# Kernel optimization log

Measured on AMD Instinct MI355X. Metric: run time of the kernel, lower is better.

## Reference

```python
import jax, jax.numpy as jnp
import numpy as np

NUM_STAB = 0.001  # numerical_stabilizer from relu_kernel_transformation


def relu_kernel(data, proj):
    """ReLU random-feature kernel: data [B,L,H,D], proj [M,D] -> [B,L,H,M]."""
    ratio = 1.0 / jnp.sqrt(jnp.asarray(proj.shape[0], jnp.float32))
    data_dash = ratio * jnp.einsum('blhd,md->blhm', data, proj)
    return jax.nn.relu(data_dash) + NUM_STAB


def setup_inputs() -> dict:
    key = jax.random.key(0)
    k1, k2, k3, k4 = jax.random.split(key, 4)
    B, L, H, D, M = 2, 4096, 8, 64, 256
    return {
        'query': jax.random.normal(k1, (B, L, H, D), jnp.float32),
        'key_t': jax.random.normal(k2, (B, L, H, D), jnp.float32),
        'value': jax.random.normal(k3, (B, L, H, D), jnp.float32),
        'projection_matrix': jax.random.normal(k4, (M, D), jnp.float32),
    }


def reference(query, key_t, value, projection_matrix):
    # Kernel feature maps [B,L,H,M]
    qp = relu_kernel(query, projection_matrix)
    kp = relu_kernel(key_t, projection_matrix)
    # Causal path operates in [L,B,H,*] layout
    qs = jnp.transpose(qp, (1, 0, 2, 3))     # [L,B,H,M]
    ks = jnp.transpose(kp, (1, 0, 2, 3))     # [L,B,H,M]
    vs = jnp.transpose(value, (1, 0, 2, 3))  # [L,B,H,D]

    B, H, M = qs.shape[1], qs.shape[2], qs.shape[3]
    D = vs.shape[3]
    init = (jnp.zeros((B, H, M, D), qs.dtype),  # running sum of k outer v
            jnp.zeros((B, H, M), qs.dtype))     # running sum of k

    def step(carry, inp):
        kv_sum, k_sum = carry
        q, k, v = inp  # [B,H,M], [B,H,M], [B,H,D]
        kv_sum = kv_sum + k[..., None] * v[..., None, :]
        k_sum = k_sum + k
        num = jnp.einsum('bhmd,bhm->bhd', kv_sum, q)  # causal numerator step
        den = jnp.einsum('bhm,bhm->bh', q, k_sum)     # causal denominator step
        return (kv_sum, k_sum), (num, den)

    _, (num, den) = jax.lax.scan(step, init, (qs, ks, vs))  # num [L,B,H,D], den [L,B,H]
    den = den[..., None]
    den = jnp.where(den <= 0.0, jnp.ones_like(den), den)
    out = num / den                      # [L,B,H,D]
    return jnp.transpose(out, (1, 0, 2, 3))  # [B,L,H,D]
```

## Files before the change

kernel.cpp:

```cpp
#include <hip/hip_runtime.h>
#include <hip/hip_bf16.h>


#define B_   2
#define L_   4096
#define H_   8
#define D_   64
#define M_   256
#define T_   128
#define C_   (L_ / T_)
#define NBH  (B_ * H_)
#define RATIO 0.0625f
#define STAB  0.001f
#define SVT  136
#define SQS  72

typedef __attribute__((ext_vector_type(8))) short short8;
typedef __attribute__((ext_vector_type(4))) float floatx4;

#define MFMA16(a, b, c) __builtin_amdgcn_mfma_f32_16x16x32_bf16(a, b, c, 0, 0, 0)

__device__ inline unsigned short f2bf(float x) {
    union { float f; unsigned u; } v; v.f = x;
    unsigned r = v.u + 0x7FFF + ((v.u >> 16) & 1);
    return (unsigned short)(r >> 16);
}
__device__ inline unsigned pack2bf(float a, float b) {
    __hip_bfloat162 h = __float22bfloat162_rn(make_float2(a, b));
    unsigned u; __builtin_memcpy(&u, &h, 4);
    return u;
}
__device__ inline short8 ldg8_bfs(const float* p) {
    float4 a = *(const float4*)p;
    float4 b = *(const float4*)(p + 4);
    short8 r;
    r[0] = (short)f2bf(a.x * RATIO); r[1] = (short)f2bf(a.y * RATIO);
    r[2] = (short)f2bf(a.z * RATIO); r[3] = (short)f2bf(a.w * RATIO);
    r[4] = (short)f2bf(b.x * RATIO); r[5] = (short)f2bf(b.y * RATIO);
    r[6] = (short)f2bf(b.z * RATIO); r[7] = (short)f2bf(b.w * RATIO);
    return r;
}

__global__ __launch_bounds__(256, 2)
void prep_kernel(const float* __restrict__ val, const float* __restrict__ proj,
                 unsigned short* __restrict__ VTg, unsigned short* __restrict__ Pbf) {
    const int c = blockIdx.x, bh = blockIdx.y;
    const int b = bh / H_, h = bh % H_;
    const int tid = threadIdx.x;
    __shared__ __align__(16) unsigned short VT[64 * SVT];

    const size_t rowstr = H_ * D_;
    const size_t base = ((size_t)b * L_ + (size_t)c * T_) * rowstr + (size_t)h * D_;

    for (int i = tid; i < T_ * 16; i += 256) {
        int t = i >> 4, d4 = (i & 15) * 4;
        float4 vv = *(const float4*)(val + base + (size_t)t * rowstr + d4);
        VT[(d4 + 0) * SVT + t] = f2bf(vv.x);
        VT[(d4 + 1) * SVT + t] = f2bf(vv.y);
        VT[(d4 + 2) * SVT + t] = f2bf(vv.z);
        VT[(d4 + 3) * SVT + t] = f2bf(vv.w);
    }
    __syncthreads();
    unsigned short* vout = VTg + ((size_t)bh * C_ + c) * (D_ * T_);
    for (int i = tid; i < D_ * 16; i += 256) {
        int d = i >> 4, tt = (i & 15) * 8;
        *(uint4*)(vout + d * T_ + tt) = *(const uint4*)&VT[d * SVT + tt];
    }
    if (c == 0) {
        int i = bh * 256 + tid;
        float4 pv = *(const float4*)(proj + (size_t)i * 4);
        uint2 o; o.x = pack2bf(pv.x, pv.y); o.y = pack2bf(pv.z, pv.w);
        *(uint2*)(Pbf + (size_t)i * 4) = o;
    }
}

__global__ __launch_bounds__(512, 1)
void scan_kernel(const float* __restrict__ key,
                 const unsigned short* __restrict__ VTg,
                 const unsigned short* __restrict__ Pbf,
                 unsigned short* __restrict__ S, float* __restrict__ Z) {
    const int mq = blockIdx.x, bh = blockIdx.y, dh = blockIdx.z;
    const int b = bh / H_, h = bh % H_;
    const int tid = threadIdx.x;
    const int w = tid >> 6, lane = tid & 63;
    const int l15 = lane & 15, quad = lane >> 4;

    __shared__ __align__(16) unsigned short KpT[2][32 * SVT];
    __shared__ float zP[2][4][32];

    const size_t rowstr = H_ * D_;
    const size_t khead = (size_t)b * L_ * rowstr + (size_t)h * D_;

    if (w < 4) {
        short8 pf[2][2];
#pragma unroll
        for (int ct = 0; ct < 2; ++ct)
#pragma unroll
            for (int kk = 0; kk < 2; ++kk)
                pf[ct][kk] = *(const short8*)(Pbf + (size_t)(mq * 32 + ct * 16 + l15) * D_
                                              + kk * 32 + quad * 8);
        short8 kf[2][2];
#pragma unroll
        for (int rt = 0; rt < 2; ++rt)
#pragma unroll
            for (int kk = 0; kk < 2; ++kk)
                kf[rt][kk] = ldg8_bfs(key + khead
                                      + (size_t)(32 * w + rt * 16 + l15) * rowstr
                                      + kk * 32 + quad * 8);
#pragma unroll
        for (int ct = 0; ct < 2; ++ct) {
            float zpart = 0.f;
#pragma unroll
            for (int rt = 0; rt < 2; ++rt) {
                floatx4 a = {0.f, 0.f, 0.f, 0.f};
                a = MFMA16(kf[rt][0], pf[ct][0], a);
                a = MFMA16(kf[rt][1], pf[ct][1], a);
                float k0 = fmaxf(a[0], 0.f) + STAB;
                float k1 = fmaxf(a[1], 0.f) + STAB;
                float k2 = fmaxf(a[2], 0.f) + STAB;
                float k3 = fmaxf(a[3], 0.f) + STAB;
                zpart += (k0 + k1) + (k2 + k3);
                uint2 pk; pk.x = pack2bf(k0, k1); pk.y = pack2bf(k2, k3);
                *(uint2*)&KpT[0][(ct * 16 + l15) * SVT + 32 * w + rt * 16 + quad * 4] = pk;
            }
            zpart += __shfl_xor(zpart, 16, 64);
            zpart += __shfl_xor(zpart, 32, 64);
            if (quad == 0) zP[0][w][ct * 16 + l15] = zpart;
        }
#pragma unroll
        for (int rt = 0; rt < 2; ++rt)
#pragma unroll
            for (int kk = 0; kk < 2; ++kk)
                kf[rt][kk] = ldg8_bfs(key + khead + (size_t)T_ * rowstr
                                      + (size_t)(32 * w + rt * 16 + l15) * rowstr
                                      + kk * 32 + quad * 8);
        __syncthreads();
        for (int c = 0; c < C_; ++c) {
            const int buf = c & 1;
            if (c + 1 < C_) {
#pragma unroll
                for (int ct = 0; ct < 2; ++ct) {
                    float zpart = 0.f;
#pragma unroll
                    for (int rt = 0; rt < 2; ++rt) {
                        floatx4 a = {0.f, 0.f, 0.f, 0.f};
                        a = MFMA16(kf[rt][0], pf[ct][0], a);
                        a = MFMA16(kf[rt][1], pf[ct][1], a);
                        float k0 = fmaxf(a[0], 0.f) + STAB;
                        float k1 = fmaxf(a[1], 0.f) + STAB;
                        float k2 = fmaxf(a[2], 0.f) + STAB;
                        float k3 = fmaxf(a[3], 0.f) + STAB;
                        zpart += (k0 + k1) + (k2 + k3);
                        uint2 pk; pk.x = pack2bf(k0, k1); pk.y = pack2bf(k2, k3);
                        *(uint2*)&KpT[buf ^ 1][(ct * 16 + l15) * SVT
                                               + 32 * w + rt * 16 + quad * 4] = pk;
                    }
                    zpart += __shfl_xor(zpart, 16, 64);
                    zpart += __shfl_xor(zpart, 32, 64);
                    if (quad == 0) zP[buf ^ 1][w][ct * 16 + l15] = zpart;
                }
                if (c + 2 < C_) {
                    const size_t kb2 = khead + (size_t)(c + 2) * T_ * rowstr;
#pragma unroll
                    for (int rt = 0; rt < 2; ++rt)
#pragma unroll
                        for (int kk = 0; kk < 2; ++kk)
                            kf[rt][kk] = ldg8_bfs(key + kb2
                                                  + (size_t)(32 * w + rt * 16 + l15) * rowstr
                                                  + kk * 32 + quad * 8);
                }
            }
            __syncthreads();
        }
    } else {
        const int w4 = w - 4;
        const int dt = w4 & 1, ct2 = w4 >> 1;
        const int vrow = dh * 32 + dt * 16 + l15;
        const int drow0 = dh * 32 + dt * 16 + quad * 4;
        const int mcol = mq * 32 + ct2 * 16 + l15;
        const unsigned short* vhead = VTg + (size_t)bh * C_ * (D_ * T_);

        floatx4 acc = {0.f, 0.f, 0.f, 0.f};
        float zreg = 0.f;
        short8 vf[4];
#pragma unroll
        for (int k4 = 0; k4 < 4; ++k4)
            vf[k4] = *(const short8*)(vhead + (size_t)vrow * T_ + k4 * 32 + quad * 8);
        __syncthreads();
        for (int c = 0; c < C_; ++c) {
            const int buf = c & 1;
            unsigned short* Sp = S + ((size_t)bh * C_ + c) * (M_ * D_);
#pragma unroll
            for (int r = 0; r < 4; ++r)
                Sp[(size_t)(drow0 + r) * M_ + mcol] = f2bf(acc[r]);
            if (w == 4 && dh == 0 && lane < 32) {
                float zs = zP[buf][0][lane] + zP[buf][1][lane]
                         + zP[buf][2][lane] + zP[buf][3][lane];
                Z[((size_t)bh * C_ + c) * M_ + mq * 32 + lane] = zreg;
                zreg += zs;
            }
            short8 vn[4];
            if (c + 1 < C_) {
                const unsigned short* vb2 = vhead + (size_t)(c + 1) * (D_ * T_);
#pragma unroll
                for (int k4 = 0; k4 < 4; ++k4)
                    vn[k4] = *(const short8*)(vb2 + (size_t)vrow * T_ + k4 * 32 + quad * 8);
            }
#pragma unroll
            for (int k4 = 0; k4 < 4; ++k4) {
                short8 kb = *(const short8*)&KpT[buf][(ct2 * 16 + l15) * SVT
                                                      + k4 * 32 + quad * 8];
                acc = MFMA16(vf[k4], kb, acc);
            }
            if (c + 1 < C_) {
#pragma unroll
                for (int k4 = 0; k4 < 4; ++k4) vf[k4] = vn[k4];
            }
            __syncthreads();
        }
    }
}

__global__ __launch_bounds__(512, 2)
void phase3_kernel(const float* __restrict__ q, const float* __restrict__ key,
                   const unsigned short* __restrict__ VTg,
                   const unsigned short* __restrict__ Pbf,
                   const unsigned short* __restrict__ S, const float* __restrict__ Z,
                   float* __restrict__ out) {
    const int c = blockIdx.x, bh = blockIdx.y;
    const int b = bh / H_, h = bh % H_;
    const int tid = threadIdx.x;
    const int w = tid >> 6, lane = tid & 63;
    const int l15 = lane & 15, quad = lane >> 4;

    __shared__ __align__(16) unsigned short KpL[T_ * SVT];
    __shared__ __align__(16) unsigned short QpS[8 * 16 * SQS];

    const size_t rowstr = H_ * D_;
    const size_t base = ((size_t)b * L_ + (size_t)c * T_) * rowstr + (size_t)h * D_;
    const unsigned short* Sp = S + (size_t)(bh * C_ + c) * (M_ * D_);
    const float* Zp = Z + (size_t)(bh * C_ + c) * M_;
    const unsigned short* Vc = VTg + ((size_t)bh * C_ + c) * (D_ * T_);

    short8 qf[2], kf[2];
#pragma unroll
    for (int kk = 0; kk < 2; ++kk) {
        size_t ro = base + (size_t)(16 * w + l15) * rowstr + kk * 32 + quad * 8;
        qf[kk] = ldg8_bfs(q + ro);
        kf[kk] = ldg8_bfs(key + ro);
    }

    unsigned short* myQp = QpS + w * 16 * SQS;
    floatx4 num[4];
    floatx4 Aacc[8];
#pragma unroll
    for (int dt = 0; dt < 4; ++dt) { floatx4 z4 = {0.f,0.f,0.f,0.f}; num[dt] = z4; }
#pragma unroll
    for (int ct = 0; ct < 8; ++ct) { floatx4 z4 = {0.f,0.f,0.f,0.f}; Aacc[ct] = z4; }
    float dz[4] = {0.f, 0.f, 0.f, 0.f};

    for (int hh = 0; hh < 2; ++hh) {
        short8 qa[4];
#pragma unroll
        for (int fgl = 0; fgl < 2; ++fgl) {
            const int fg = 2 * hh + fgl;
#pragma unroll
            for (int ct = 0; ct < 4; ++ct) {
                const unsigned short* pp = Pbf + (size_t)(fg * 64 + ct * 16 + l15) * D_;
                short8 pf0 = *(const short8*)(pp + quad * 8);
                short8 pf1 = *(const short8*)(pp + 32 + quad * 8);
                floatx4 aq = {0.f, 0.f, 0.f, 0.f};
                aq = MFMA16(qf[0], pf0, aq);
                aq = MFMA16(qf[1], pf1, aq);
                floatx4 ak = {0.f, 0.f, 0.f, 0.f};
                ak = MFMA16(kf[0], pf0, ak);
                ak = MFMA16(kf[1], pf1, ak);
                const int mloc = fgl * 64 + ct * 16 + l15;
                float zv = Zp[hh * 128 + mloc];
#pragma unroll
                for (int r = 0; r < 4; ++r) {
                    float qpv = fmaxf(aq[r], 0.f) + STAB;
                    float kpv = fmaxf(ak[r], 0.f) + STAB;
                    myQp[(quad * 4 + r) * SQS + ct * 16 + l15] = f2bf(qpv);
                    KpL[(size_t)(16 * w + quad * 4 + r) * SVT + mloc] = f2bf(kpv);
                    dz[r] = fmaf(qpv, zv, dz[r]);
                }
            }
#pragma unroll
            for (int kk = 0; kk < 2; ++kk)
                qa[fgl * 2 + kk] = *(const short8*)&myQp[l15 * SQS + kk * 32 + quad * 8];
        }
#pragma unroll
        for (int dt = 0; dt < 4; ++dt)
#pragma unroll
            for (int kc = 0; kc < 4; ++kc) {
                short8 sb = *(const short8*)(Sp + (size_t)(dt * 16 + l15) * M_
                                             + hh * 128 + kc * 32 + quad * 8);
                num[dt] = MFMA16(qa[kc], sb, num[dt]);
            }
        __syncthreads();
#pragma unroll
        for (int ct = 0; ct < 8; ++ct) {
            if (ct <= w) {
#pragma unroll
                for (int kc = 0; kc < 4; ++kc) {
                    short8 kb = *(const short8*)&KpL[(size_t)(ct * 16 + l15) * SVT
                                                     + kc * 32 + quad * 8];
                    Aacc[ct] = MFMA16(qa[kc], kb, Aacc[ct]);
                }
            }
        }
        __syncthreads();
    }
#pragma unroll
    for (int r = 0; r < 4; ++r) {
        dz[r] += __shfl_xor(dz[r], 1, 64);
        dz[r] += __shfl_xor(dz[r], 2, 64);
        dz[r] += __shfl_xor(dz[r], 4, 64);
        dz[r] += __shfl_xor(dz[r], 8, 64);
    }

    unsigned short* AmL = KpL;
    float da[4] = {0.f, 0.f, 0.f, 0.f};
#pragma unroll
    for (int ct = 0; ct < 8; ++ct)
#pragma unroll
        for (int r = 0; r < 4; ++r) {
            float av = Aacc[ct][r];
            if (ct > w || (ct == w && l15 > quad * 4 + r)) av = 0.f;
            AmL[(size_t)(16 * w + quad * 4 + r) * SVT + ct * 16 + l15] = f2bf(av);
            da[r] += av;
        }
#pragma unroll
    for (int r = 0; r < 4; ++r) {
        da[r] += __shfl_xor(da[r], 1, 64);
        da[r] += __shfl_xor(da[r], 2, 64);
        da[r] += __shfl_xor(da[r], 4, 64);
        da[r] += __shfl_xor(da[r], 8, 64);
    }

    for (int k4 = 0; k4 <= (w >> 1); ++k4) {
        short8 am = *(const short8*)&AmL[(size_t)(16 * w + l15) * SVT
                                         + k4 * 32 + quad * 8];
#pragma unroll
        for (int dt = 0; dt < 4; ++dt) {
            short8 vb = *(const short8*)(Vc + (size_t)(dt * 16 + l15) * T_
                                         + k4 * 32 + quad * 8);
            num[dt] = MFMA16(am, vb, num[dt]);
        }
    }

#pragma unroll
    for (int r = 0; r < 4; ++r) {
        float den = da[r] + dz[r];
        if (den <= 0.f) den = 1.f;
        float inv = 1.f / den;
        int t = 16 * w + quad * 4 + r;
#pragma unroll
        for (int dt = 0; dt < 4; ++dt)
            out[base + (size_t)t * rowstr + dt * 16 + l15] = num[dt][r] * inv;
    }
}

extern "C" void kernel_launch(void* const* d_in, const int* in_sizes, int n_in,
                              void* d_out, int out_size, void* d_ws, size_t ws_size,
                              hipStream_t stream) {
    const float* q    = (const float*)d_in[0];
    const float* k    = (const float*)d_in[1];
    const float* v    = (const float*)d_in[2];
    const float* proj = (const float*)d_in[3];
    float* out = (float*)d_out;

    const size_t nS = (size_t)NBH * C_ * D_ * M_;
    const size_t nZ = (size_t)NBH * C_ * M_;
    const size_t nV = (size_t)NBH * C_ * D_ * T_;
    unsigned short* S   = (unsigned short*)d_ws;
    float*          Z   = (float*)(S + nS);
    unsigned short* VTg = (unsigned short*)(Z + nZ);
    unsigned short* Pbf = VTg + nV;

    prep_kernel<<<dim3(C_, NBH), dim3(256), 0, stream>>>(v, proj, VTg, Pbf);
    scan_kernel<<<dim3(8, NBH, 2), dim3(512), 0, stream>>>(k, VTg, Pbf, S, Z);
    phase3_kernel<<<dim3(C_, NBH), dim3(512), 0, stream>>>(q, k, VTg, Pbf, S, Z, out);
}
```

Baseline: 183.1 us.

## Replace serial chunk scan with parallel per-chunk partials plus prefix-sum kernel

The sequential scan kernel that walked all chunks per (m-slice, bh) block is replaced by a chunk kernel. It computes each chunk's K^T V outer-product sum and k-sum independently in parallel across all chunks, writing fp32 partials to workspace. A separate prefix kernel then does an exclusive cumulative sum over chunks to produce S (bf16) and Z. This removes the serial dependency chain and its low grid parallelism, at the cost of extra fp32 workspace traffic (partials written and re-read) and one more launch.

```diff
diff --git a/kernel.cpp b/kernel.cpp
--- a/kernel.cpp
+++ b/kernel.cpp
@@ -40,19 +40,35 @@
     r[6] = (short)f2bf(b.z * RATIO); r[7] = (short)f2bf(b.w * RATIO);
     return r;
 }
-
-__global__ __launch_bounds__(256, 2)
-void prep_kernel(const float* __restrict__ val, const float* __restrict__ proj,
-                 unsigned short* __restrict__ VTg, unsigned short* __restrict__ Pbf) {
+__device__ inline short8 ldg8_bf(const float* p) {
+    float4 a = *(const float4*)p;
+    float4 b = *(const float4*)(p + 4);
+    short8 r;
+    r[0] = (short)f2bf(a.x); r[1] = (short)f2bf(a.y);
+    r[2] = (short)f2bf(a.z); r[3] = (short)f2bf(a.w);
+    r[4] = (short)f2bf(b.x); r[5] = (short)f2bf(b.y);
+    r[6] = (short)f2bf(b.z); r[7] = (short)f2bf(b.w);
+    return r;
+}
+
+__global__ __launch_bounds__(512, 2)
+void chunk_kernel(const float* __restrict__ key, const float* __restrict__ val,
+                  const float* __restrict__ proj,
+                  unsigned short* __restrict__ VTg, unsigned short* __restrict__ Pbf,
+                  float* __restrict__ Ppart, float* __restrict__ Zpart) {
     const int c = blockIdx.x, bh = blockIdx.y;
     const int b = bh / H_, h = bh % H_;
     const int tid = threadIdx.x;
+    const int w = tid >> 6, lane = tid & 63;
+    const int l15 = lane & 15, quad = lane >> 4;
+
     __shared__ __align__(16) unsigned short VT[64 * SVT];
+    __shared__ __align__(16) unsigned short KpT[128 * SVT];
 
     const size_t rowstr = H_ * D_;
     const size_t base = ((size_t)b * L_ + (size_t)c * T_) * rowstr + (size_t)h * D_;
 
-    for (int i = tid; i < T_ * 16; i += 256) {
+    for (int i = tid; i < T_ * 16; i += 512) {
         int t = i >> 4, d4 = (i & 15) * 4;
         float4 vv = *(const float4*)(val + base + (size_t)t * rowstr + d4);
         VT[(d4 + 0) * SVT + t] = f2bf(vv.x);
@@ -62,161 +78,96 @@
     }
     __syncthreads();
     unsigned short* vout = VTg + ((size_t)bh * C_ + c) * (D_ * T_);
-    for (int i = tid; i < D_ * 16; i += 256) {
+    for (int i = tid; i < D_ * 16; i += 512) {
         int d = i >> 4, tt = (i & 15) * 8;
         *(uint4*)(vout + d * T_ + tt) = *(const uint4*)&VT[d * SVT + tt];
     }
-    if (c == 0) {
+    if (c == 0 && tid < 256) {
         int i = bh * 256 + tid;
         float4 pv = *(const float4*)(proj + (size_t)i * 4);
         uint2 o; o.x = pack2bf(pv.x, pv.y); o.y = pack2bf(pv.z, pv.w);
         *(uint2*)(Pbf + (size_t)i * 4) = o;
     }
-}
-
-__global__ __launch_bounds__(512, 1)
-void scan_kernel(const float* __restrict__ key,
-                 const unsigned short* __restrict__ VTg,
-                 const unsigned short* __restrict__ Pbf,
-                 unsigned short* __restrict__ S, float* __restrict__ Z) {
-    const int mq = blockIdx.x, bh = blockIdx.y, dh = blockIdx.z;
-    const int b = bh / H_, h = bh % H_;
-    const int tid = threadIdx.x;
-    const int w = tid >> 6, lane = tid & 63;
-    const int l15 = lane & 15, quad = lane >> 4;
-
-    __shared__ __align__(16) unsigned short KpT[2][32 * SVT];
-    __shared__ float zP[2][4][32];
-
-    const size_t rowstr = H_ * D_;
-    const size_t khead = (size_t)b * L_ * rowstr + (size_t)h * D_;
-
-    if (w < 4) {
-        short8 pf[2][2];
-#pragma unroll
-        for (int ct = 0; ct < 2; ++ct)
-#pragma unroll
-            for (int kk = 0; kk < 2; ++kk)
-                pf[ct][kk] = *(const short8*)(Pbf + (size_t)(mq * 32 + ct * 16 + l15) * D_
-                                              + kk * 32 + quad * 8);
-        short8 kf[2][2];
-#pragma unroll
-        for (int rt = 0; rt < 2; ++rt)
-#pragma unroll
-            for (int kk = 0; kk < 2; ++kk)
-                kf[rt][kk] = ldg8_bfs(key + khead
-                                      + (size_t)(32 * w + rt * 16 + l15) * rowstr
-                                      + kk * 32 + quad * 8);
-#pragma unroll
-        for (int ct = 0; ct < 2; ++ct) {
-            float zpart = 0.f;
-#pragma unroll
-            for (int rt = 0; rt < 2; ++rt) {
-                floatx4 a = {0.f, 0.f, 0.f, 0.f};
-                a = MFMA16(kf[rt][0], pf[ct][0], a);
-                a = MFMA16(kf[rt][1], pf[ct][1], a);
-                float k0 = fmaxf(a[0], 0.f) + STAB;
-                float k1 = fmaxf(a[1], 0.f) + STAB;
-                float k2 = fmaxf(a[2], 0.f) + STAB;
-                float k3 = fmaxf(a[3], 0.f) + STAB;
-                zpart += (k0 + k1) + (k2 + k3);
-                uint2 pk; pk.x = pack2bf(k0, k1); pk.y = pack2bf(k2, k3);
-                *(uint2*)&KpT[0][(ct * 16 + l15) * SVT + 32 * w + rt * 16 + quad * 4] = pk;
-            }
-            zpart += __shfl_xor(zpart, 16, 64);
-            zpart += __shfl_xor(zpart, 32, 64);
-            if (quad == 0) zP[0][w][ct * 16 + l15] = zpart;
-        }
-#pragma unroll
-        for (int rt = 0; rt < 2; ++rt)
-#pragma unroll
-            for (int kk = 0; kk < 2; ++kk)
-                kf[rt][kk] = ldg8_bfs(key + khead + (size_t)T_ * rowstr
-                                      + (size_t)(32 * w + rt * 16 + l15) * rowstr
-                                      + kk * 32 + quad * 8);
+
+    float* Pp = Ppart + ((size_t)bh * C_ + c) * (D_ * M_);
+
+    for (int half = 0; half < 2; ++half) {
+        const int mrow = half * 128 + w * 16 + l15;
+        short8 pf0 = ldg8_bf(proj + (size_t)mrow * D_ + quad * 8);
+        short8 pf1 = ldg8_bf(proj + (size_t)mrow * D_ + 32 + quad * 8);
+        if (half) __syncthreads();
+        float zp = 0.f;
+#pragma unroll
+        for (int rt = 0; rt < 8; ++rt) {
+            const float* kr = key + base + (size_t)(rt * 16 + l15) * rowstr;
+            short8 kf0 = ldg8_bfs(kr + quad * 8);
+            short8 kf1 = ldg8_bfs(kr + 32 + quad * 8);
+            floatx4 a = {0.f, 0.f, 0.f, 0.f};
+            a = MFMA16(kf0, pf0, a);
+            a = MFMA16(kf1, pf1, a);
+            float k0 = fmaxf(a[0], 0.f) + STAB;
+            float k1 = fmaxf(a[1], 0.f) + STAB;
+            float k2 = fmaxf(a[2], 0.f) + STAB;
+            float k3 = fmaxf(a[3], 0.f) + STAB;
+            zp += (k0 + k1) + (k2 + k3);
+            uint2 pk; pk.x = pack2bf(k0, k1); pk.y = pack2bf(k2, k3);
+            *(uint2*)&KpT[(w * 16 + l15) * SVT + rt * 16 + quad * 4] = pk;
+        }
+        zp += __shfl_xor(zp, 16, 64);
+        zp += __shfl_xor(zp, 32, 64);
+        if (quad == 0)
+            Zpart[((size_t)bh * C_ + c) * M_ + mrow] = zp;
         __syncthreads();
-        for (int c = 0; c < C_; ++c) {
-            const int buf = c & 1;
-            if (c + 1 < C_) {
-#pragma unroll
-                for (int ct = 0; ct < 2; ++ct) {
-                    float zpart = 0.f;
-#pragma unroll
-                    for (int rt = 0; rt < 2; ++rt) {
-                        floatx4 a = {0.f, 0.f, 0.f, 0.f};
-                        a = MFMA16(kf[rt][0], pf[ct][0], a);
-                        a = MFMA16(kf[rt][1], pf[ct][1], a);
-                        float k0 = fmaxf(a[0], 0.f) + STAB;
-                        float k1 = fmaxf(a[1], 0.f) + STAB;
-                        float k2 = fmaxf(a[2], 0.f) + STAB;
-                        float k3 = fmaxf(a[3], 0.f) + STAB;
-                        zpart += (k0 + k1) + (k2 + k3);
-                        uint2 pk; pk.x = pack2bf(k0, k1); pk.y = pack2bf(k2, k3);
-                        *(uint2*)&KpT[buf ^ 1][(ct * 16 + l15) * SVT
-                                               + 32 * w + rt * 16 + quad * 4] = pk;
-                    }
-                    zpart += __shfl_xor(zpart, 16, 64);
-                    zpart += __shfl_xor(zpart, 32, 64);
-                    if (quad == 0) zP[buf ^ 1][w][ct * 16 + l15] = zpart;
-                }
-                if (c + 2 < C_) {
-                    const size_t kb2 = khead + (size_t)(c + 2) * T_ * rowstr;
-#pragma unroll
-                    for (int rt = 0; rt < 2; ++rt)
-#pragma unroll
-                        for (int kk = 0; kk < 2; ++kk)
-                            kf[rt][kk] = ldg8_bfs(key + kb2
-                                                  + (size_t)(32 * w + rt * 16 + l15) * rowstr
-                                                  + kk * 32 + quad * 8);
-                }
-            }
-            __syncthreads();
-        }
-    } else {
-        const int w4 = w - 4;
-        const int dt = w4 & 1, ct2 = w4 >> 1;
-        const int vrow = dh * 32 + dt * 16 + l15;
-        const int drow0 = dh * 32 + dt * 16 + quad * 4;
-        const int mcol = mq * 32 + ct2 * 16 + l15;
-        const unsigned short* vhead = VTg + (size_t)bh * C_ * (D_ * T_);
-
-        floatx4 acc = {0.f, 0.f, 0.f, 0.f};
-        float zreg = 0.f;
+
+        const int dt_w = w >> 1;
+        const int mt0 = (w & 1) * 4;
         short8 vf[4];
 #pragma unroll
         for (int k4 = 0; k4 < 4; ++k4)
-            vf[k4] = *(const short8*)(vhead + (size_t)vrow * T_ + k4 * 32 + quad * 8);
-        __syncthreads();
-        for (int c = 0; c < C_; ++c) {
-            const int buf = c & 1;
-            unsigned short* Sp = S + ((size_t)bh * C_ + c) * (M_ * D_);
-#pragma unroll
-            for (int r = 0; r < 4; ++r)
-                Sp[(size_t)(drow0 + r) * M_ + mcol] = f2bf(acc[r]);
-            if (w == 4 && dh == 0 && lane < 32) {
-                float zs = zP[buf][0][lane] + zP[buf][1][lane]
-                         + zP[buf][2][lane] + zP[buf][3][lane];
-                Z[((size_t)bh * C_ + c) * M_ + mq * 32 + lane] = zreg;
-                zreg += zs;
-            }
-            short8 vn[4];
-            if (c + 1 < C_) {
-                const unsigned short* vb2 = vhead + (size_t)(c + 1) * (D_ * T_);
-#pragma unroll
-                for (int k4 = 0; k4 < 4; ++k4)
-                    vn[k4] = *(const short8*)(vb2 + (size_t)vrow * T_ + k4 * 32 + quad * 8);
-            }
+            vf[k4] = *(const short8*)&VT[(dt_w * 16 + l15) * SVT + k4 * 32 + quad * 8];
+#pragma unroll
+        for (int mt = 0; mt < 4; ++mt) {
+            floatx4 acc = {0.f, 0.f, 0.f, 0.f};
 #pragma unroll
             for (int k4 = 0; k4 < 4; ++k4) {
-                short8 kb = *(const short8*)&KpT[buf][(ct2 * 16 + l15) * SVT
-                                                      + k4 * 32 + quad * 8];
+                short8 kb = *(const short8*)&KpT[((mt0 + mt) * 16 + l15) * SVT
+                                                 + k4 * 32 + quad * 8];
                 acc = MFMA16(vf[k4], kb, acc);
             }
-            if (c + 1 < C_) {
-#pragma unroll
-                for (int k4 = 0; k4 < 4; ++k4) vf[k4] = vn[k4];
-            }
-            __syncthreads();
+            const int mcol = half * 128 + (mt0 + mt) * 16 + l15;
+#pragma unroll
+            for (int r = 0; r < 4; ++r)
+                Pp[(size_t)(dt_w * 16 + quad * 4 + r) * M_ + mcol] = acc[r];
+        }
+    }
+}
+
+__global__ __launch_bounds__(256, 4)
+void prefix_kernel(const float* __restrict__ Ppart, const float* __restrict__ Zpart,
+                   unsigned short* __restrict__ S, float* __restrict__ Z) {
+    const int g = blockIdx.x, bh = blockIdx.y;
+    const int tid = threadIdx.x;
+    if (g < 16) {
+        const size_t dm = ((size_t)g * 256 + tid) * 4;
+        const float* Pp = Ppart + (size_t)bh * C_ * (D_ * M_) + dm;
+        unsigned short* Sp = S + (size_t)bh * C_ * (D_ * M_) + dm;
+        float4 acc = make_float4(0.f, 0.f, 0.f, 0.f);
+#pragma unroll 4
+        for (int c = 0; c < C_; ++c) {
+            float4 p = *(const float4*)(Pp + (size_t)c * (D_ * M_));
+            uint2 o; o.x = pack2bf(acc.x, acc.y); o.y = pack2bf(acc.z, acc.w);
+            *(uint2*)(Sp + (size_t)c * (D_ * M_)) = o;
+            acc.x += p.x; acc.y += p.y; acc.z += p.z; acc.w += p.w;
+        }
+    } else {
+        const float* Zp = Zpart + (size_t)bh * C_ * M_ + tid;
+        float* Zo = Z + (size_t)bh * C_ * M_ + tid;
+        float acc = 0.f;
+#pragma unroll 4
+        for (int c = 0; c < C_; ++c) {
+            float z = Zp[(size_t)c * M_];
+            Zo[(size_t)c * M_] = acc;
+            acc += z;
         }
     }
 }
@@ -374,12 +325,14 @@
     const size_t nS = (size_t)NBH * C_ * D_ * M_;
     const size_t nZ = (size_t)NBH * C_ * M_;
     const size_t nV = (size_t)NBH * C_ * D_ * T_;
-    unsigned short* S   = (unsigned short*)d_ws;
-    float*          Z   = (float*)(S + nS);
-    unsigned short* VTg = (unsigned short*)(Z + nZ);
-    unsigned short* Pbf = VTg + nV;
-
-    prep_kernel<<<dim3(C_, NBH), dim3(256), 0, stream>>>(v, proj, VTg, Pbf);
-    scan_kernel<<<dim3(8, NBH, 2), dim3(512), 0, stream>>>(k, VTg, Pbf, S, Z);
+    unsigned short* S     = (unsigned short*)d_ws;
+    float*          Z     = (float*)(S + nS);
+    unsigned short* VTg   = (unsigned short*)(Z + nZ);
+    unsigned short* Pbf   = VTg + nV;
+    float*          Ppart = (float*)(Pbf + (size_t)M_ * D_);
+    float*          Zpart = Ppart + nS;
+
+    chunk_kernel<<<dim3(C_, NBH), dim3(512), 0, stream>>>(k, v, proj, VTg, Pbf, Ppart, Zpart);
+    prefix_kernel<<<dim3(17, NBH), dim3(256), 0, stream>>>(Ppart, Zpart, S, Z);
     phase3_kernel<<<dim3(C_, NBH), dim3(512), 0, stream>>>(q, k, VTg, Pbf, S, Z, out);
 }
```

Measured after the change: 168.9 us. -7.7%, faster.
